# Kernel tuning notes

Measured on AMD Instinct MI355X. Metric: run time of the kernel, lower is better.

The kernel has to match this reference:

```python
import jax, jax.numpy as jnp
import numpy as np

HEAD_SIZE = 64


def setup_inputs() -> dict:
    key = jax.random.key(0)
    ks = jax.random.split(key, 7)
    B, S, D, H = 4, 2048, 1024, HEAD_SIZE
    return {
        "key_input": jax.random.normal(ks[0], (B, S, D), dtype=jnp.float32),
        "query_input": jax.random.normal(ks[1], (B, S, D), dtype=jnp.float32),
        "value_input": jax.random.normal(ks[2], (B, S, D), dtype=jnp.float32),
        "mask": jax.random.randint(ks[3], (B, S, S), 0, 2).astype(jnp.bool_),
        "Wq": jax.random.normal(ks[4], (D, H), dtype=jnp.float32) * (D ** -0.5),
        "Wk": jax.random.normal(ks[5], (D, H), dtype=jnp.float32) * (D ** -0.5),
        "Wv": jax.random.normal(ks[6], (D, H), dtype=jnp.float32) * (D ** -0.5),
    }


def reference(key_input, query_input, value_input, mask, Wq, Wk, Wv):
    # q,k,v: [B, S, H]
    q = query_input @ Wq
    k = key_input @ Wk
    v = value_input @ Wv
    scale = HEAD_SIZE ** -0.5
    # scores: [B, S, S]
    wei = jnp.einsum("bqh,bkh->bqk", q, k) * scale
    wei = jnp.where(mask, -jnp.inf, wei)
    wei = jax.nn.softmax(wei, axis=-1)
    out = jnp.einsum("bqk,bkh->bqh", wei, v)  # [B, S, H]
    return out
```

## Files before the change

### kernel.cpp

```cpp
#include <hip/hip_runtime.h>
#include <hip/hip_bf16.h>
#include <math.h>

#define BATCH 4
#define SEQ   2048
#define DIM   1024
#define HEAD  64
#define NCHUNK ((BATCH * SEQ * SEQ) / 64)

typedef __attribute__((ext_vector_type(8))) short bf16x8;
typedef __attribute__((ext_vector_type(4))) short bf16x4;
typedef __attribute__((ext_vector_type(4))) float f32x4;

static __device__ __forceinline__ short f2bf(float f) {
    __hip_bfloat16 h = __float2bfloat16(f);
    return *reinterpret_cast<short*>(&h);
}

__global__ __launch_bounds__(256) void wconv_detect_kernel(
    const float* __restrict__ Wq, const float* __restrict__ Wk, const float* __restrict__ Wv,
    short* __restrict__ Wt, const unsigned int* __restrict__ mask_u32,
    int* __restrict__ mflag)
{
    const int which = blockIdx.y;
    const float* __restrict__ W = (which == 0) ? Wq : (which == 1) ? Wk : Wv;
    short* __restrict__ Wtw = Wt + (size_t)which * HEAD * DIM;

    const int h  = threadIdx.x & 63;
    const int k0 = blockIdx.x * 64 + (threadIdx.x >> 6) * 16;
    #pragma unroll
    for (int j = 0; j < 16; ++j) {
        int k = k0 + j;
        Wtw[((size_t)(k >> 5) * 64 + h) * 32 + (k & 31)] =
            f2bf(W[(size_t)k * HEAD + h]);
    }

    if (blockIdx.x == 0 && blockIdx.y == 0 && threadIdx.x < 64) {
        int lane = threadIdx.x;
        bool weird = false;
        for (int i = lane; i < 1024; i += 64) weird |= (mask_u32[i] > 1u);
        unsigned long long b = __ballot(weird);
        if (lane == 0) *mflag = (b != 0ull) ? 1 : 0;
    }
}

__global__ __launch_bounds__(256, 5) void prep_kernel(
    const float* __restrict__ Xq, const float* __restrict__ Xk, const float* __restrict__ Xv,
    const short* __restrict__ Wt, const void* __restrict__ mask,
    const int* __restrict__ mflag, unsigned long long* __restrict__ packed,
    short* __restrict__ Q, short* __restrict__ K, short* __restrict__ Vt)
{
    const int bx  = blockIdx.x;
    const int tid = threadIdx.x;
    const int lane = tid & 63;
    const int w    = tid >> 6;

    if (bx < 512) {
        const int gw = bx * 4 + w;
        const int c0 = gw * 128;
        const int useByte = *mflag;
        if (useByte) {
            const unsigned char* mb = (const unsigned char*)mask;
            for (int i = 0; i < 8; ++i) {
                unsigned char v[16];
                #pragma unroll
                for (int j = 0; j < 16; ++j)
                    v[j] = mb[(size_t)(c0 + i * 16 + j) * 64 + lane];
                #pragma unroll
                for (int j = 0; j < 16; ++j) {
                    unsigned long long bb = __ballot(v[j] != 0);
                    if (lane == 0) packed[c0 + i * 16 + j] = bb;
                }
            }
        } else {
            const unsigned int* mw = (const unsigned int*)mask;
            for (int i = 0; i < 8; ++i) {
                unsigned int v[16];
                #pragma unroll
                for (int j = 0; j < 16; ++j)
                    v[j] = mw[(size_t)(c0 + i * 16 + j) * 64 + lane];
                #pragma unroll
                for (int j = 0; j < 16; ++j) {
                    unsigned long long bb = __ballot(v[j] != 0);
                    if (lane == 0) packed[c0 + i * 16 + j] = bb;
                }
            }
        }
        return;
    }

    __shared__ float O_lds[4][32][64];

    const int pi    = bx - 512;
    const int which = pi >> 8;
    const int row0  = (pi & 255) * 32;
    const float* __restrict__ X = (which == 0) ? Xq : (which == 1) ? Xk : Xv;
    const short* __restrict__ Wtw = Wt + (size_t)which * HEAD * DIM;

    const int g = lane >> 4;
    const int c = lane & 15;

    const float* __restrict__ Xp0 = X + (size_t)(row0 + c) * DIM + w * 256 + g * 8;
    const float* __restrict__ Xp1 = Xp0 + (size_t)16 * DIM;
    const short* __restrict__ Wp  = Wtw + (size_t)(w * 8) * 2048 + c * 32 + g * 8;

    f32x4 acc0[4], acc1[4];
    #pragma unroll
    for (int n = 0; n < 4; ++n) { acc0[n] = (f32x4)0.0f; acc1[n] = (f32x4)0.0f; }

    #pragma unroll
    for (int half = 0; half < 2; ++half) {
        f32x4 xa0[4], xb0[4], xa1[4], xb1[4];
        #pragma unroll
        for (int s = 0; s < 4; ++s) {
            xa0[s] = *(const f32x4*)(Xp0 + half * 128 + s * 32);
            xb0[s] = *(const f32x4*)(Xp0 + half * 128 + s * 32 + 4);
            xa1[s] = *(const f32x4*)(Xp1 + half * 128 + s * 32);
            xb1[s] = *(const f32x4*)(Xp1 + half * 128 + s * 32 + 4);
        }
        bf16x8 wf[16];
        #pragma unroll
        for (int s = 0; s < 4; ++s)
            #pragma unroll
            for (int n = 0; n < 4; ++n)
                wf[s * 4 + n] = *(const bf16x8*)(Wp + (size_t)(half * 4 + s) * 2048
                                                 + n * 512);
        #pragma unroll
        for (int s = 0; s < 4; ++s) {
            bf16x8 a0, a1;
            a0[0]=f2bf(xa0[s][0]); a0[1]=f2bf(xa0[s][1]); a0[2]=f2bf(xa0[s][2]); a0[3]=f2bf(xa0[s][3]);
            a0[4]=f2bf(xb0[s][0]); a0[5]=f2bf(xb0[s][1]); a0[6]=f2bf(xb0[s][2]); a0[7]=f2bf(xb0[s][3]);
            a1[0]=f2bf(xa1[s][0]); a1[1]=f2bf(xa1[s][1]); a1[2]=f2bf(xa1[s][2]); a1[3]=f2bf(xa1[s][3]);
            a1[4]=f2bf(xb1[s][0]); a1[5]=f2bf(xb1[s][1]); a1[6]=f2bf(xb1[s][2]); a1[7]=f2bf(xb1[s][3]);
            #pragma unroll
            for (int n = 0; n < 4; ++n) {
                acc0[n] = __builtin_amdgcn_mfma_f32_16x16x32_bf16(a0, wf[s * 4 + n],
                                                                  acc0[n], 0, 0, 0);
                acc1[n] = __builtin_amdgcn_mfma_f32_16x16x32_bf16(a1, wf[s * 4 + n],
                                                                  acc1[n], 0, 0, 0);
            }
        }
    }

    #pragma unroll
    for (int n = 0; n < 4; ++n)
        #pragma unroll
        for (int r = 0; r < 4; ++r) {
            O_lds[w][g * 4 + r][n * 16 + c]      = acc0[n][r];
            O_lds[w][16 + g * 4 + r][n * 16 + c] = acc1[n][r];
        }
    __syncthreads();

    if (which < 2) {
        short* dst = (which == 0) ? Q : K;
        const int trow = tid >> 3, c8 = (tid & 7) * 8;
        f32x4 sA = *(const f32x4*)&O_lds[0][trow][c8];
        f32x4 sB = *(const f32x4*)&O_lds[0][trow][c8 + 4];
        #pragma unroll
        for (int i = 1; i < 4; ++i) {
            f32x4 tA = *(const f32x4*)&O_lds[i][trow][c8];
            f32x4 tB = *(const f32x4*)&O_lds[i][trow][c8 + 4];
            #pragma unroll
            for (int j = 0; j < 4; ++j) { sA[j] += tA[j]; sB[j] += tB[j]; }
        }
        bf16x8 pk;
        #pragma unroll
        for (int j = 0; j < 4; ++j) { pk[j] = f2bf(sA[j]); pk[4 + j] = f2bf(sB[j]); }
        *(bf16x8*)&dst[(size_t)(row0 + trow) * HEAD + c8] = pk;
    } else {
        const int h = tid & 63, r8 = (tid >> 6) * 8;
        const int b = row0 >> 11, sb = row0 & (SEQ - 1);
        bf16x8 pk;
        #pragma unroll
        for (int j = 0; j < 8; ++j) {
            float v = O_lds[0][r8 + j][h] + O_lds[1][r8 + j][h]
                    + O_lds[2][r8 + j][h] + O_lds[3][r8 + j][h];
            pk[j] = f2bf(v);
        }
        *(bf16x8*)&Vt[((size_t)(b * HEAD + h)) * SEQ + sb + r8] = pk;
    }
}

__global__ __launch_bounds__(512, 2) void attn_kernel(
    const short* __restrict__ Q, const short* __restrict__ K, const short* __restrict__ Vt,
    const unsigned int* __restrict__ packed, float* __restrict__ out)
{
    const int bi    = blockIdx.x;
    const int b     = bi & 3;
    const int qbase = (bi >> 2) * 32;
    const int tid  = threadIdx.x;
    const int lane = tid & 63;
    const int w    = tid >> 6;
    const int g    = lane >> 4;
    const int c    = lane & 15;

    const short* Qb = Q  + (size_t)(b * SEQ + qbase) * HEAD;
    const short* Kb = K  + (size_t)b * SEQ * HEAD;
    const short* Vb = Vt + (size_t)b * HEAD * SEQ;

    __shared__ __align__(16) unsigned char smem[32768 + 1024];
    short (*P_lds)[2][4][16][8] = (short (*)[2][4][16][8])smem;
    float (*O_lds)[16][64]      = (float (*)[16][64])smem;
    float (*M_lds)[16] = (float (*)[16])(smem + 32768);
    float (*L_lds)[16] = (float (*)[16])(smem + 32768 + 512);

    const unsigned int* pw0 = packed + (size_t)(b * SEQ + qbase + c) * 64 + w * 8;
    unsigned int mw0[8], mw1[8];
    #pragma unroll
    for (int i = 0; i < 8; ++i) { mw0[i] = pw0[i]; mw1[i] = pw0[16 * 64 + i]; }

    bf16x8 qb0 = *(const bf16x8*)&Qb[c * HEAD + g * 8];
    bf16x8 qb1 = *(const bf16x8*)&Qb[c * HEAD + 32 + g * 8];
    bf16x8 qc0 = *(const bf16x8*)&Qb[(16 + c) * HEAD + g * 8];
    bf16x8 qc1 = *(const bf16x8*)&Qb[(16 + c) * HEAD + 32 + g * 8];

    float m0 = -INFINITY, l0 = 0.0f, m1 = -INFINITY, l1 = 0.0f;
    f32x4 o0[4], o1[4];
    #pragma unroll
    for (int n = 0; n < 4; ++n) { o0[n] = (f32x4)0.0f; o1[n] = (f32x4)0.0f; }

    const float scale = 0.125f;
    const float LOG2E = 1.44269504088896340736f;

    for (int i = 0; i < 8; ++i) {
        const int kt = w * 8 + i;
        const short* Kt = Kb + (size_t)kt * 32 * HEAD;

        bf16x8 vb[4];
        #pragma unroll
        for (int n = 0; n < 4; ++n)
            vb[n] = *(const bf16x8*)&Vb[(size_t)(n * 16 + c) * SEQ + kt * 32 + g * 8];

        bf16x8 ka00 = *(const bf16x8*)&Kt[c * HEAD + g * 8];
        bf16x8 ka01 = *(const bf16x8*)&Kt[c * HEAD + 32 + g * 8];
        bf16x8 ka10 = *(const bf16x8*)&Kt[(16 + c) * HEAD + g * 8];
        bf16x8 ka11 = *(const bf16x8*)&Kt[(16 + c) * HEAD + 32 + g * 8];

        f32x4 s0t0 = (f32x4)0.0f, s1t0 = (f32x4)0.0f;
        s0t0 = __builtin_amdgcn_mfma_f32_16x16x32_bf16(ka00, qb0, s0t0, 0, 0, 0);
        s0t0 = __builtin_amdgcn_mfma_f32_16x16x32_bf16(ka01, qb1, s0t0, 0, 0, 0);
        s1t0 = __builtin_amdgcn_mfma_f32_16x16x32_bf16(ka10, qb0, s1t0, 0, 0, 0);
        s1t0 = __builtin_amdgcn_mfma_f32_16x16x32_bf16(ka11, qb1, s1t0, 0, 0, 0);
        f32x4 s0t1 = (f32x4)0.0f, s1t1 = (f32x4)0.0f;
        s0t1 = __builtin_amdgcn_mfma_f32_16x16x32_bf16(ka00, qc0, s0t1, 0, 0, 0);
        s0t1 = __builtin_amdgcn_mfma_f32_16x16x32_bf16(ka01, qc1, s0t1, 0, 0, 0);
        s1t1 = __builtin_amdgcn_mfma_f32_16x16x32_bf16(ka10, qc0, s1t1, 0, 0, 0);
        s1t1 = __builtin_amdgcn_mfma_f32_16x16x32_bf16(ka11, qc1, s1t1, 0, 0, 0);

        #pragma unroll
        for (int t = 0; t < 2; ++t) {
            const f32x4 s0 = t ? s0t1 : s0t0;
            const f32x4 s1 = t ? s1t1 : s1t0;
            const unsigned int mw32 = t ? mw1[i] : mw0[i];
            float& m_run = t ? m1 : m0;
            float& l_run = t ? l1 : l0;
            f32x4* o = t ? o1 : o0;

            float sv[8];
            #pragma unroll
            for (int r = 0; r < 4; ++r) {
                sv[r]     = ((mw32 >> (g * 4 + r)) & 1u)      ? -INFINITY : s0[r] * scale;
                sv[4 + r] = ((mw32 >> (16 + g * 4 + r)) & 1u) ? -INFINITY : s1[r] * scale;
            }

            float mx = fmaxf(fmaxf(fmaxf(sv[0], sv[1]), fmaxf(sv[2], sv[3])),
                             fmaxf(fmaxf(sv[4], sv[5]), fmaxf(sv[6], sv[7])));
            mx = fmaxf(mx, __shfl_xor(mx, 16));
            mx = fmaxf(mx, __shfl_xor(mx, 32));

            if (!__all(mx <= m_run + 8.0f)) {
                float mn = fmaxf(m_run, mx);
                float cf = (m_run == mn) ? 1.0f : exp2f((m_run - mn) * LOG2E);
                float cfq[4];
                #pragma unroll
                for (int r = 0; r < 4; ++r)
                    cfq[r] = __shfl(cf, (lane & 48) | (g * 4 + r));
                #pragma unroll
                for (int n = 0; n < 4; ++n)
                    #pragma unroll
                    for (int r = 0; r < 4; ++r) o[n][r] *= cfq[r];
                l_run *= cf;
                m_run = mn;
            }

            const float mb = m_run * LOG2E;
            float p[8];
            #pragma unroll
            for (int j = 0; j < 8; ++j)
                p[j] = (sv[j] <= -1e37f) ? 0.0f : exp2f(sv[j] * LOG2E - mb);
            float rs = ((p[0] + p[1]) + (p[2] + p[3])) + ((p[4] + p[5]) + (p[6] + p[7]));
            rs += __shfl_xor(rs, 16);
            rs += __shfl_xor(rs, 32);
            l_run += rs;

            bf16x4 p0v, p1v;
            #pragma unroll
            for (int r = 0; r < 4; ++r) { p0v[r] = f2bf(p[r]); p1v[r] = f2bf(p[4 + r]); }
            *(bf16x4*)&P_lds[w][t][g >> 1][c][(g & 1) * 4]       = p0v;
            *(bf16x4*)&P_lds[w][t][2 + (g >> 1)][c][(g & 1) * 4] = p1v;
            bf16x8 pa = *(bf16x8*)&P_lds[w][t][g][c][0];
            #pragma unroll
            for (int n = 0; n < 4; ++n)
                o[n] = __builtin_amdgcn_mfma_f32_16x16x32_bf16(pa, vb[n], o[n], 0, 0, 0);
        }
    }

    const int row  = tid >> 5;
    const int col0 = (tid & 31) * 2;
    float* Ob0 = out + (size_t)(b * SEQ + qbase + row) * HEAD;
    float* Ob1 = out + (size_t)(b * SEQ + qbase + 16 + row) * HEAD;

    #pragma unroll
    for (int t = 0; t < 2; ++t) {
        __syncthreads();
        const f32x4* o = t ? o1 : o0;
        #pragma unroll
        for (int n = 0; n < 4; ++n)
            #pragma unroll
            for (int r = 0; r < 4; ++r)
                O_lds[w][g * 4 + r][n * 16 + c] = o[n][r];
        if (lane < 16) {
            M_lds[w][lane] = t ? m1 : m0;
            L_lds[w][lane] = t ? l1 : l0;
        }
        __syncthreads();

        float M = -INFINITY;
        #pragma unroll
        for (int i = 0; i < 8; ++i) M = fmaxf(M, M_lds[i][row]);
        float L = 0.0f, a0 = 0.0f, a1 = 0.0f;
        #pragma unroll
        for (int i = 0; i < 8; ++i) {
            float wgt = exp2f((M_lds[i][row] - M) * LOG2E);
            L  += L_lds[i][row] * wgt;
            a0 += O_lds[i][row][col0]     * wgt;
            a1 += O_lds[i][row][col0 + 1] * wgt;
        }
        float inv = 1.0f / L;
        float* Ob = t ? Ob1 : Ob0;
        Ob[col0]     = a0 * inv;
        Ob[col0 + 1] = a1 * inv;
    }
}

extern "C" void kernel_launch(void* const* d_in, const int* in_sizes, int n_in,
                              void* d_out, int out_size, void* d_ws, size_t ws_size,
                              hipStream_t stream)
{
    const float* key_in   = (const float*)d_in[0];
    const float* query_in = (const float*)d_in[1];
    const float* value_in = (const float*)d_in[2];
    const void*  mask     = d_in[3];
    const float* Wq = (const float*)d_in[4];
    const float* Wk = (const float*)d_in[5];
    const float* Wv = (const float*)d_in[6];

    char* ws = (char*)d_ws;
    short* Qw  = (short*)ws;
    short* Kw  = Qw + (size_t)BATCH * SEQ * HEAD;
    short* Vtw = Kw + (size_t)BATCH * SEQ * HEAD;
    unsigned long long* packed =
        (unsigned long long*)(ws + (size_t)3 * BATCH * SEQ * HEAD * sizeof(short));
    short* Wt  = (short*)((char*)packed + (size_t)NCHUNK * 8);
    int* mflag = (int*)((char*)Wt + (size_t)3 * HEAD * DIM * sizeof(short));

    wconv_detect_kernel<<<dim3(16, 3), 256, 0, stream>>>(
        Wq, Wk, Wv, Wt, (const unsigned int*)mask, mflag);

    prep_kernel<<<1280, 256, 0, stream>>>(
        query_in, key_in, value_in, Wt, mask, mflag, packed, Qw, Kw, Vtw);

    attn_kernel<<<256, 512, 0, stream>>>(
        Qw, Kw, Vtw, (const unsigned int*)packed, (float*)d_out);
}
```

Baseline: 57.44 us.

## Fuse mask bit-packing into attention kernel via LDS instead of prep pass

Mask packing moves out of the prep kernel into the attention kernel. Each attention block reads its own 32-row mask slice, ballot-packs it into LDS bitmasks, and reads mask words from LDS in the inner loop. This removes the global packed-mask buffer's write and re-read and shrinks the prep grid. In exchange, attention blocks take on the full mask read latency up front before any compute, and each uses 8 KB more LDS.

Result: slower. 58.62 us (+2.1%).

```diff
diff --git a/kernel.cpp b/kernel.cpp
--- a/kernel.cpp
+++ b/kernel.cpp
@@ -6,7 +6,6 @@
 #define SEQ   2048
 #define DIM   1024
 #define HEAD  64
-#define NCHUNK ((BATCH * SEQ * SEQ) / 64)
 
 typedef __attribute__((ext_vector_type(8))) short bf16x8;
 typedef __attribute__((ext_vector_type(4))) short bf16x4;
@@ -46,52 +45,16 @@
 
 __global__ __launch_bounds__(256, 5) void prep_kernel(
     const float* __restrict__ Xq, const float* __restrict__ Xk, const float* __restrict__ Xv,
-    const short* __restrict__ Wt, const void* __restrict__ mask,
-    const int* __restrict__ mflag, unsigned long long* __restrict__ packed,
+    const short* __restrict__ Wt,
     short* __restrict__ Q, short* __restrict__ K, short* __restrict__ Vt)
 {
-    const int bx  = blockIdx.x;
-    const int tid = threadIdx.x;
+    const int tid  = threadIdx.x;
     const int lane = tid & 63;
     const int w    = tid >> 6;
 
-    if (bx < 512) {
-        const int gw = bx * 4 + w;
-        const int c0 = gw * 128;
-        const int useByte = *mflag;
-        if (useByte) {
-            const unsigned char* mb = (const unsigned char*)mask;
-            for (int i = 0; i < 8; ++i) {
-                unsigned char v[16];
-                #pragma unroll
-                for (int j = 0; j < 16; ++j)
-                    v[j] = mb[(size_t)(c0 + i * 16 + j) * 64 + lane];
-                #pragma unroll
-                for (int j = 0; j < 16; ++j) {
-                    unsigned long long bb = __ballot(v[j] != 0);
-                    if (lane == 0) packed[c0 + i * 16 + j] = bb;
-                }
-            }
-        } else {
-            const unsigned int* mw = (const unsigned int*)mask;
-            for (int i = 0; i < 8; ++i) {
-                unsigned int v[16];
-                #pragma unroll
-                for (int j = 0; j < 16; ++j)
-                    v[j] = mw[(size_t)(c0 + i * 16 + j) * 64 + lane];
-                #pragma unroll
-                for (int j = 0; j < 16; ++j) {
-                    unsigned long long bb = __ballot(v[j] != 0);
-                    if (lane == 0) packed[c0 + i * 16 + j] = bb;
-                }
-            }
-        }
-        return;
-    }
-
     __shared__ float O_lds[4][32][64];
 
-    const int pi    = bx - 512;
+    const int pi    = blockIdx.x;
     const int which = pi >> 8;
     const int row0  = (pi & 255) * 32;
     const float* __restrict__ X = (which == 0) ? Xq : (which == 1) ? Xk : Xv;
@@ -183,7 +146,8 @@
 
 __global__ __launch_bounds__(512, 2) void attn_kernel(
     const short* __restrict__ Q, const short* __restrict__ K, const short* __restrict__ Vt,
-    const unsigned int* __restrict__ packed, float* __restrict__ out)
+    const void* __restrict__ mask, const int* __restrict__ mflag,
+    float* __restrict__ out)
 {
     const int bi    = blockIdx.x;
     const int b     = bi & 3;
@@ -198,16 +162,63 @@
     const short* Kb = K  + (size_t)b * SEQ * HEAD;
     const short* Vb = Vt + (size_t)b * HEAD * SEQ;
 
-    __shared__ __align__(16) unsigned char smem[32768 + 1024];
+    __shared__ __align__(16) unsigned char smem[32768 + 1024 + 8192];
     short (*P_lds)[2][4][16][8] = (short (*)[2][4][16][8])smem;
     float (*O_lds)[16][64]      = (float (*)[16][64])smem;
     float (*M_lds)[16] = (float (*)[16])(smem + 32768);
     float (*L_lds)[16] = (float (*)[16])(smem + 32768 + 512);
-
-    const unsigned int* pw0 = packed + (size_t)(b * SEQ + qbase + c) * 64 + w * 8;
-    unsigned int mw0[8], mw1[8];
-    #pragma unroll
-    for (int i = 0; i < 8; ++i) { mw0[i] = pw0[i]; mw1[i] = pw0[16 * 64 + i]; }
+    unsigned int* Mbits = (unsigned int*)(smem + 33792);
+
+    {
+        const int useByte = *mflag;
+        const size_t mrow0 = (size_t)(b * SEQ + qbase) * SEQ;
+        if (useByte) {
+            const unsigned char* mb = (const unsigned char*)mask + mrow0;
+            #pragma unroll
+            for (int bt = 0; bt < 8; ++bt) {
+                unsigned char v[16];
+                #pragma unroll
+                for (int j = 0; j < 16; ++j) {
+                    int idx = w * 128 + bt * 16 + j;
+                    int row = idx >> 5, w64 = idx & 31;
+                    v[j] = mb[(size_t)row * SEQ + w64 * 64 + lane];
+                }
+                #pragma unroll
+                for (int j = 0; j < 16; ++j) {
+                    int idx = w * 128 + bt * 16 + j;
+                    int row = idx >> 5, w64 = idx & 31;
+                    unsigned long long bb = __ballot(v[j] != 0);
+                    if (lane == 0) {
+                        Mbits[(2 * w64) * 32 + row]     = (unsigned int)bb;
+                        Mbits[(2 * w64 + 1) * 32 + row] = (unsigned int)(bb >> 32);
+                    }
+                }
+            }
+        } else {
+            const unsigned int* mw = (const unsigned int*)mask + mrow0;
+            #pragma unroll
+            for (int bt = 0; bt < 8; ++bt) {
+                unsigned int v[16];
+                #pragma unroll
+                for (int j = 0; j < 16; ++j) {
+                    int idx = w * 128 + bt * 16 + j;
+                    int row = idx >> 5, w64 = idx & 31;
+                    v[j] = mw[(size_t)row * SEQ + w64 * 64 + lane];
+                }
+                #pragma unroll
+                for (int j = 0; j < 16; ++j) {
+                    int idx = w * 128 + bt * 16 + j;
+                    int row = idx >> 5, w64 = idx & 31;
+                    unsigned long long bb = __ballot(v[j] != 0);
+                    if (lane == 0) {
+                        Mbits[(2 * w64) * 32 + row]     = (unsigned int)bb;
+                        Mbits[(2 * w64 + 1) * 32 + row] = (unsigned int)(bb >> 32);
+                    }
+                }
+            }
+        }
+    }
+    __syncthreads();
 
     bf16x8 qb0 = *(const bf16x8*)&Qb[c * HEAD + g * 8];
     bf16x8 qb1 = *(const bf16x8*)&Qb[c * HEAD + 32 + g * 8];
@@ -251,7 +262,7 @@
         for (int t = 0; t < 2; ++t) {
             const f32x4 s0 = t ? s0t1 : s0t0;
             const f32x4 s1 = t ? s1t1 : s1t0;
-            const unsigned int mw32 = t ? mw1[i] : mw0[i];
+            const unsigned int mw32 = Mbits[(w * 8 + i) * 32 + t * 16 + c];
             float& m_run = t ? m1 : m0;
             float& l_run = t ? l1 : l0;
             f32x4* o = t ? o1 : o0;
@@ -359,17 +370,15 @@
     short* Qw  = (short*)ws;
     short* Kw  = Qw + (size_t)BATCH * SEQ * HEAD;
     short* Vtw = Kw + (size_t)BATCH * SEQ * HEAD;
-    unsigned long long* packed =
-        (unsigned long long*)(ws + (size_t)3 * BATCH * SEQ * HEAD * sizeof(short));
-    short* Wt  = (short*)((char*)packed + (size_t)NCHUNK * 8);
+    short* Wt  = Vtw + (size_t)BATCH * SEQ * HEAD;
     int* mflag = (int*)((char*)Wt + (size_t)3 * HEAD * DIM * sizeof(short));
 
     wconv_detect_kernel<<<dim3(16, 3), 256, 0, stream>>>(
         Wq, Wk, Wv, Wt, (const unsigned int*)mask, mflag);
 
-    prep_kernel<<<1280, 256, 0, stream>>>(
-        query_in, key_in, value_in, Wt, mask, mflag, packed, Qw, Kw, Vtw);
+    prep_kernel<<<768, 256, 0, stream>>>(
+        query_in, key_in, value_in, Wt, Qw, Kw, Vtw);
 
     attn_kernel<<<256, 512, 0, stream>>>(
-        Qw, Kw, Vtw, (const unsigned int*)packed, (float*)d_out);
-}
+        Qw, Kw, Vtw, mask, mflag, (float*)d_out);
+}
```
